# Kernel optimization log

Hardware: AMD Instinct MI355X
Metric: run time of the kernel (lower is better)

## Reference

```python
import jax, jax.numpy as jnp
import numpy as np

TAU = 1.0
EPS = 1e-8  # F.cosine_similarity default eps


def _normalize(v):
    n = jnp.sqrt(jnp.sum(v * v, axis=-1, keepdims=True))
    return v / jnp.maximum(n, EPS)


def _compute_cl(X, Y):
    # cosine-sim matrix via normalize + matmul (same math as broadcasted
    # F.cosine_similarity, without the (bs,bs,hidden) intermediate)
    S = _normalize(X) @ _normalize(Y).T            # (bs, bs), S[i,j] = cos(X_i, Y_j)
    E = jnp.exp(S / TAU)                            # (bs, bs)
    pos = jnp.diagonal(E)                           # (bs,) exp(diag/tau)
    neg = jnp.sum(E, axis=0) - pos                  # (bs,) column sums minus diagonal
    return (-jnp.log(pos / neg))[:, None]           # (bs, 1) — torch's view(bs, -1)


def setup_inputs() -> dict:
    key = jax.random.key(0)
    kx, ky = jax.random.split(key)
    X = jax.random.normal(kx, (8192, 2048), dtype=jnp.float32)
    Y = jax.random.normal(ky, (8192, 2048), dtype=jnp.float32)
    return {"X": X, "Y": Y}


def reference(X, Y):
    return _compute_cl(X, Y) + _compute_cl(Y, X)
```

## Files before the change

kernel.cpp:

```cpp
#include <hip/hip_runtime.h>
#include <hip/hip_bf16.h>
#include <math.h>

typedef float f32x4 __attribute__((ext_vector_type(4)));
typedef int   i32x4 __attribute__((ext_vector_type(4)));
typedef int   i32x8 __attribute__((ext_vector_type(8)));

#define BSZ 8192
#define DIM 2048
#define NTILE 64
#define NKG 16

#define SCALE_I32 0x79797979


__device__ __forceinline__ unsigned f2fp4(float v) {
  float a = fabsf(v);
  unsigned s = (__float_as_uint(v) >> 31) << 3;
  unsigned m = (a < 0.25f) ? 0u
             : (a < 0.75f) ? 1u
             : (a < 1.25f) ? 2u
             : (a < 1.75f) ? 3u
             : (a < 2.5f)  ? 4u
             : (a < 3.5f)  ? 5u
             : (a < 5.0f)  ? 6u : 7u;
  return s | m;
}

__global__ void __launch_bounds__(256) k_prep(const float* __restrict__ X,
                                              const float* __restrict__ Y,
                                              unsigned char* __restrict__ Xq,
                                              unsigned char* __restrict__ Yq,
                                              float* __restrict__ dg) {
  const int row = blockIdx.x;
  const int tid = threadIdx.x;
  const float4* xp = (const float4*)(X + (size_t)row * DIM);
  const float4* yp = (const float4*)(Y + (size_t)row * DIM);
  float4 x0 = xp[tid * 2], x1 = xp[tid * 2 + 1];
  float4 y0 = yp[tid * 2], y1 = yp[tid * 2 + 1];
  float sxx = x0.x*x0.x + x0.y*x0.y + x0.z*x0.z + x0.w*x0.w
            + x1.x*x1.x + x1.y*x1.y + x1.z*x1.z + x1.w*x1.w;
  float syy = y0.x*y0.x + y0.y*y0.y + y0.z*y0.z + y0.w*y0.w
            + y1.x*y1.x + y1.y*y1.y + y1.z*y1.z + y1.w*y1.w;
  float sxy = x0.x*y0.x + x0.y*y0.y + x0.z*y0.z + x0.w*y0.w
            + x1.x*y1.x + x1.y*y1.y + x1.z*y1.z + x1.w*y1.w;
#pragma unroll
  for (int m = 32; m >= 1; m >>= 1) {
    sxx += __shfl_xor(sxx, m);
    syy += __shfl_xor(syy, m);
    sxy += __shfl_xor(sxy, m);
  }
  __shared__ float sh[3][4];
  if ((tid & 63) == 0) {
    sh[0][tid >> 6] = sxx; sh[1][tid >> 6] = syy; sh[2][tid >> 6] = sxy;
  }
  __syncthreads();
  float xx = sh[0][0] + sh[0][1] + sh[0][2] + sh[0][3];
  float yy = sh[1][0] + sh[1][1] + sh[1][2] + sh[1][3];
  float xy = sh[2][0] + sh[2][1] + sh[2][2] + sh[2][3];
  float nx = fmaxf(sqrtf(xx), 1e-8f);
  float ny = fmaxf(sqrtf(yy), 1e-8f);
  float ix = 64.0f / nx, iy = 64.0f / ny;
  float vx[8] = {x0.x, x0.y, x0.z, x0.w, x1.x, x1.y, x1.z, x1.w};
  float vy[8] = {y0.x, y0.y, y0.z, y0.w, y1.x, y1.y, y1.z, y1.w};
  unsigned ux = 0, uy = 0;
#pragma unroll
  for (int i = 0; i < 8; ++i) {
    ux |= f2fp4(vx[i] * ix) << (4 * i);
    uy |= f2fp4(vy[i] * iy) << (4 * i);
  }
  const unsigned kkg = tid >> 4;
  const unsigned hi4 = (tid >> 2) & 3;
  const unsigned byt = (tid & 3) * 4;
  const unsigned R = row >> 4, lo16 = row & 15;
  const size_t addr = (((size_t)(kkg << 9) + R) << 10) + (hi4 * 16 + lo16) * 16 + byt;
  *(unsigned*)(Xq + addr) = ux;
  *(unsigned*)(Yq + addr) = uy;
  if (tid == 0) dg[row] = xy / (nx * ny);
}

__global__ void __launch_bounds__(256) k_gemm(const unsigned char* __restrict__ Xq,
                                              const unsigned char* __restrict__ Yq,
                                              float* __restrict__ rowpart,
                                              float* __restrict__ colpart) {
  const int bm = blockIdx.x & (NTILE - 1);
  const int bn = blockIdx.x >> 6;
  const int tileRow = bm * 128;
  const int tileCol = bn * 128;

  __shared__ float rsum2[2][128];
  __shared__ float csum2[2][128];

  const int tid = threadIdx.x;
  const int lane = tid & 63;
  const int w = tid >> 6;
  const int wr = w >> 1;
  const int wc = w & 1;
  const int lo = lane & 15;
  const int hi = lane >> 4;

  f32x4 acc[4][4];
#pragma unroll
  for (int m = 0; m < 4; ++m)
#pragma unroll
    for (int n = 0; n < 4; ++n) acc[m][n] = (f32x4){0.f, 0.f, 0.f, 0.f};

  const unsigned char* Ab = Xq + (((size_t)(bm * 8 + wr * 4)) << 10) + lane * 16;
  const unsigned char* Bb = Yq + (((size_t)(bn * 8 + wc * 4)) << 10) + lane * 16;

#define LOADF(da, db, g) do {                                                  \
    const unsigned char* pa_ = Ab + ((size_t)(g) << 19);                       \
    const unsigned char* pb_ = Bb + ((size_t)(g) << 19);                       \
    da[0] = *(const i32x4*)(pa_);                                              \
    da[1] = *(const i32x4*)(pa_ + 1024);                                       \
    da[2] = *(const i32x4*)(pa_ + 2048);                                       \
    da[3] = *(const i32x4*)(pa_ + 3072);                                       \
    db[0] = *(const i32x4*)(pb_);                                              \
    db[1] = *(const i32x4*)(pb_ + 1024);                                       \
    db[2] = *(const i32x4*)(pb_ + 2048);                                       \
    db[3] = *(const i32x4*)(pb_ + 3072);                                       \
  } while (0)

#define MM(aa, bb) do {                                                        \
    _Pragma("unroll")                                                          \
    for (int m_ = 0; m_ < 4; ++m_) {                                           \
      i32x8 av_ = {aa[m_][0], aa[m_][1], aa[m_][2], aa[m_][3], 0, 0, 0, 0};    \
      _Pragma("unroll")                                                        \
      for (int n_ = 0; n_ < 4; ++n_) {                                         \
        i32x8 bv_ = {bb[n_][0], bb[n_][1], bb[n_][2], bb[n_][3], 0, 0, 0, 0};  \
        acc[m_][n_] = __builtin_amdgcn_mfma_scale_f32_16x16x128_f8f6f4(        \
            av_, bv_, acc[m_][n_], 4, 4, 0, SCALE_I32, 0, SCALE_I32);          \
      }                                                                        \
    }                                                                          \
  } while (0)

  i32x4 a0[4], b0[4], a1[4], b1[4];
  LOADF(a0, b0, 0);
  for (int g = 0; g < NKG; g += 2) {
    LOADF(a1, b1, g + 1);
    MM(a0, b0);
    if (g + 2 < NKG) LOADF(a0, b0, g + 2);
    MM(a1, b1);
  }
#undef LOADF
#undef MM

  float rp[4][4];
  float cp[4];
#pragma unroll
  for (int m = 0; m < 4; ++m)
#pragma unroll
    for (int q = 0; q < 4; ++q) rp[m][q] = 0.f;
#pragma unroll
  for (int n = 0; n < 4; ++n) cp[n] = 0.f;

#pragma unroll
  for (int m = 0; m < 4; ++m)
#pragma unroll
    for (int n = 0; n < 4; ++n)
#pragma unroll
      for (int q = 0; q < 4; ++q) {
        float e = __expf(acc[m][n][q]);
        rp[m][q] += e;
        cp[n] += e;
      }

#pragma unroll
  for (int m = 0; m < 4; ++m)
#pragma unroll
    for (int q = 0; q < 4; ++q) {
      float v = rp[m][q];
      v += __shfl_xor(v, 1);
      v += __shfl_xor(v, 2);
      v += __shfl_xor(v, 4);
      v += __shfl_xor(v, 8);
      rp[m][q] = v;
    }
#pragma unroll
  for (int n = 0; n < 4; ++n) {
    float v = cp[n];
    v += __shfl_xor(v, 16);
    v += __shfl_xor(v, 32);
    cp[n] = v;
  }

  if (lo == 0) {
#pragma unroll
    for (int m = 0; m < 4; ++m)
#pragma unroll
      for (int q = 0; q < 4; ++q)
        rsum2[wc][wr * 64 + m * 16 + hi * 4 + q] = rp[m][q];
  }
  if (hi == 0) {
#pragma unroll
    for (int n = 0; n < 4; ++n)
      csum2[wr][wc * 64 + n * 16 + lo] = cp[n];
  }
  __syncthreads();

  if (tid < 128) {
    rowpart[(size_t)bn * BSZ + tileRow + tid] = rsum2[0][tid] + rsum2[1][tid];
    colpart[(size_t)bm * BSZ + tileCol + tid] = csum2[0][tid] + csum2[1][tid];
  }
}

__global__ void __launch_bounds__(256) k_final(const float* __restrict__ rowpart,
                                               const float* __restrict__ colpart,
                                               const float* __restrict__ dg,
                                               float* __restrict__ out) {
  const int k = blockIdx.x * 256 + threadIdx.x;
  float rs = 0.f, cs = 0.f;
#pragma unroll 8
  for (int s = 0; s < NTILE; ++s) {
    rs += rowpart[(size_t)s * BSZ + k];
    cs += colpart[(size_t)s * BSZ + k];
  }
  float d = dg[k];
  float p = __expf(d);
  out[k] = logf(cs - p) + logf(rs - p) - 2.0f * d;
}

extern "C" void kernel_launch(void* const* d_in, const int* in_sizes, int n_in,
                              void* d_out, int out_size, void* d_ws, size_t ws_size,
                              hipStream_t stream) {
  const float* X = (const float*)d_in[0];
  const float* Y = (const float*)d_in[1];
  float* out = (float*)d_out;

  char* ws = (char*)d_ws;
  unsigned char* Xq = (unsigned char*)ws;
  unsigned char* Yq = (unsigned char*)(ws + (size_t)BSZ * DIM / 2);
  float* diag = (float*)(ws + (size_t)BSZ * DIM);
  float* rowpart = (float*)(ws + (size_t)BSZ * DIM + BSZ * 4);
  float* colpart = (float*)(ws + (size_t)BSZ * DIM + BSZ * 4 + (size_t)NTILE * BSZ * 4);

  k_prep<<<BSZ, 256, 0, stream>>>(X, Y, Xq, Yq, diag);
  k_gemm<<<NTILE * NTILE, 256, 0, stream>>>(Xq, Yq, rowpart, colpart);
  k_final<<<BSZ / 256, 256, 0, stream>>>(rowpart, colpart, diag, out);
}
```

Baseline: 127.7 us.

## Switch FP4 GEMM to 32x32x64 scaled MFMA with matching packed layout

Replaces the 16x16x128 scaled FP4 MFMA tiles with 32x32x64 instructions, so each wave computes a 2x2 grid of 32x32 accumulators per 128-wide K group. The prep kernel's packed FP4 layout is changed to match the new operand fragment ordering (32-row groups, K split into halves). The epilogue row/column reductions and LDS indexing are rewritten for the 16-element accumulator layout. The aim is fewer MFMA issues with larger tiles and better operand reuse per instruction. The risk is a different register footprint and a more costly row-sum shuffle pattern.

```diff
diff --git a/kernel.cpp b/kernel.cpp
--- a/kernel.cpp
+++ b/kernel.cpp
@@ -2,7 +2,7 @@
 #include <hip/hip_bf16.h>
 #include <math.h>
 
-typedef float f32x4 __attribute__((ext_vector_type(4)));
+typedef float f32x16 __attribute__((ext_vector_type(16)));
 typedef int   i32x4 __attribute__((ext_vector_type(4)));
 typedef int   i32x8 __attribute__((ext_vector_type(8)));
 
@@ -69,11 +69,12 @@
     ux |= f2fp4(vx[i] * ix) << (4 * i);
     uy |= f2fp4(vy[i] * iy) << (4 * i);
   }
-  const unsigned kkg = tid >> 4;
-  const unsigned hi4 = (tid >> 2) & 3;
-  const unsigned byt = (tid & 3) * 4;
-  const unsigned R = row >> 4, lo16 = row & 15;
-  const size_t addr = (((size_t)(kkg << 9) + R) << 10) + (hi4 * 16 + lo16) * 16 + byt;
+  const unsigned g2    = tid >> 3;
+  const unsigned khalf = (tid >> 2) & 1;
+  const unsigned byt   = (tid & 3) * 4;
+  const unsigned R32 = row >> 5, lo32 = row & 31;
+  const size_t addr = (((size_t)(g2 << 8) + R32) << 10)
+                    + (khalf * 32 + lo32) * 16 + byt;
   *(unsigned*)(Xq + addr) = ux;
   *(unsigned*)(Yq + addr) = uy;
   if (tid == 0) dg[row] = xy / (nx * ny);
@@ -96,42 +97,48 @@
   const int w = tid >> 6;
   const int wr = w >> 1;
   const int wc = w & 1;
-  const int lo = lane & 15;
-  const int hi = lane >> 4;
-
-  f32x4 acc[4][4];
-#pragma unroll
-  for (int m = 0; m < 4; ++m)
-#pragma unroll
-    for (int n = 0; n < 4; ++n) acc[m][n] = (f32x4){0.f, 0.f, 0.f, 0.f};
-
-  const unsigned char* Ab = Xq + (((size_t)(bm * 8 + wr * 4)) << 10) + lane * 16;
-  const unsigned char* Bb = Yq + (((size_t)(bn * 8 + wc * 4)) << 10) + lane * 16;
+  const int l31 = lane & 31;
+  const int hi2 = lane >> 5;
+
+  f32x16 acc[2][2];
+#pragma unroll
+  for (int mi = 0; mi < 2; ++mi)
+#pragma unroll
+    for (int ni = 0; ni < 2; ++ni)
+#pragma unroll
+      for (int q = 0; q < 16; ++q) acc[mi][ni][q] = 0.f;
+
+  const unsigned char* Ab = Xq + (((size_t)(bm * 4 + wr * 2)) << 10) + lane * 16;
+  const unsigned char* Bb = Yq + (((size_t)(bn * 4 + wc * 2)) << 10) + lane * 16;
 
 #define LOADF(da, db, g) do {                                                  \
-    const unsigned char* pa_ = Ab + ((size_t)(g) << 19);                       \
-    const unsigned char* pb_ = Bb + ((size_t)(g) << 19);                       \
+    const unsigned char* pa_ = Ab + ((size_t)(2 * (g)) << 18);                 \
+    const unsigned char* pb_ = Bb + ((size_t)(2 * (g)) << 18);                 \
     da[0] = *(const i32x4*)(pa_);                                              \
     da[1] = *(const i32x4*)(pa_ + 1024);                                       \
-    da[2] = *(const i32x4*)(pa_ + 2048);                                       \
-    da[3] = *(const i32x4*)(pa_ + 3072);                                       \
+    da[2] = *(const i32x4*)(pa_ + (1 << 18));                                  \
+    da[3] = *(const i32x4*)(pa_ + (1 << 18) + 1024);                           \
     db[0] = *(const i32x4*)(pb_);                                              \
     db[1] = *(const i32x4*)(pb_ + 1024);                                       \
-    db[2] = *(const i32x4*)(pb_ + 2048);                                       \
-    db[3] = *(const i32x4*)(pb_ + 3072);                                       \
+    db[2] = *(const i32x4*)(pb_ + (1 << 18));                                  \
+    db[3] = *(const i32x4*)(pb_ + (1 << 18) + 1024);                           \
   } while (0)
 
 #define MM(aa, bb) do {                                                        \
     _Pragma("unroll")                                                          \
-    for (int m_ = 0; m_ < 4; ++m_) {                                           \
-      i32x8 av_ = {aa[m_][0], aa[m_][1], aa[m_][2], aa[m_][3], 0, 0, 0, 0};    \
+    for (int kk_ = 0; kk_ < 2; ++kk_)                                          \
       _Pragma("unroll")                                                        \
-      for (int n_ = 0; n_ < 4; ++n_) {                                         \
-        i32x8 bv_ = {bb[n_][0], bb[n_][1], bb[n_][2], bb[n_][3], 0, 0, 0, 0};  \
-        acc[m_][n_] = __builtin_amdgcn_mfma_scale_f32_16x16x128_f8f6f4(        \
-            av_, bv_, acc[m_][n_], 4, 4, 0, SCALE_I32, 0, SCALE_I32);          \
+      for (int mi_ = 0; mi_ < 2; ++mi_) {                                      \
+        i32x8 av_ = {aa[kk_*2+mi_][0], aa[kk_*2+mi_][1],                       \
+                     aa[kk_*2+mi_][2], aa[kk_*2+mi_][3], 0, 0, 0, 0};          \
+        _Pragma("unroll")                                                      \
+        for (int ni_ = 0; ni_ < 2; ++ni_) {                                    \
+          i32x8 bv_ = {bb[kk_*2+ni_][0], bb[kk_*2+ni_][1],                     \
+                       bb[kk_*2+ni_][2], bb[kk_*2+ni_][3], 0, 0, 0, 0};        \
+          acc[mi_][ni_] = __builtin_amdgcn_mfma_scale_f32_32x32x64_f8f6f4(     \
+              av_, bv_, acc[mi_][ni_], 4, 4, 0, SCALE_I32, 0, SCALE_I32);      \
+        }                                                                      \
       }                                                                        \
-    }                                                                          \
   } while (0)
 
   i32x4 a0[4], b0[4], a1[4], b1[4];
@@ -145,56 +152,53 @@
 #undef LOADF
 #undef MM
 
-  float rp[4][4];
-  float cp[4];
-#pragma unroll
-  for (int m = 0; m < 4; ++m)
-#pragma unroll
-    for (int q = 0; q < 4; ++q) rp[m][q] = 0.f;
-#pragma unroll
-  for (int n = 0; n < 4; ++n) cp[n] = 0.f;
-
-#pragma unroll
-  for (int m = 0; m < 4; ++m)
-#pragma unroll
-    for (int n = 0; n < 4; ++n)
-#pragma unroll
-      for (int q = 0; q < 4; ++q) {
-        float e = __expf(acc[m][n][q]);
-        rp[m][q] += e;
-        cp[n] += e;
+  float rp[2][16];
+  float cp[2];
+#pragma unroll
+  for (int mi = 0; mi < 2; ++mi)
+#pragma unroll
+    for (int r = 0; r < 16; ++r) rp[mi][r] = 0.f;
+  cp[0] = 0.f; cp[1] = 0.f;
+
+#pragma unroll
+  for (int mi = 0; mi < 2; ++mi)
+#pragma unroll
+    for (int ni = 0; ni < 2; ++ni)
+#pragma unroll
+      for (int r = 0; r < 16; ++r) {
+        float e = __expf(acc[mi][ni][r]);
+        rp[mi][r] += e;
+        cp[ni] += e;
       }
 
 #pragma unroll
-  for (int m = 0; m < 4; ++m)
-#pragma unroll
-    for (int q = 0; q < 4; ++q) {
-      float v = rp[m][q];
+  for (int mi = 0; mi < 2; ++mi)
+#pragma unroll
+    for (int r = 0; r < 16; ++r) {
+      float v = rp[mi][r];
       v += __shfl_xor(v, 1);
       v += __shfl_xor(v, 2);
       v += __shfl_xor(v, 4);
       v += __shfl_xor(v, 8);
-      rp[m][q] = v;
+      v += __shfl_xor(v, 16);
+      rp[mi][r] = v;
     }
-#pragma unroll
-  for (int n = 0; n < 4; ++n) {
-    float v = cp[n];
-    v += __shfl_xor(v, 16);
-    v += __shfl_xor(v, 32);
-    cp[n] = v;
-  }
-
-  if (lo == 0) {
-#pragma unroll
-    for (int m = 0; m < 4; ++m)
-#pragma unroll
-      for (int q = 0; q < 4; ++q)
-        rsum2[wc][wr * 64 + m * 16 + hi * 4 + q] = rp[m][q];
-  }
-  if (hi == 0) {
-#pragma unroll
-    for (int n = 0; n < 4; ++n)
-      csum2[wr][wc * 64 + n * 16 + lo] = cp[n];
+  cp[0] += __shfl_xor(cp[0], 32);
+  cp[1] += __shfl_xor(cp[1], 32);
+
+  if (l31 == 0) {
+#pragma unroll
+    for (int mi = 0; mi < 2; ++mi)
+#pragma unroll
+      for (int r = 0; r < 16; ++r) {
+        int lrow = wr * 64 + mi * 32 + (r & 3) + 8 * (r >> 2) + 4 * hi2;
+        rsum2[wc][lrow] = rp[mi][r];
+      }
+  }
+  if (hi2 == 0) {
+#pragma unroll
+    for (int ni = 0; ni < 2; ++ni)
+      csum2[wr][wc * 64 + ni * 32 + l31] = cp[ni];
   }
   __syncthreads();
 
```

New measurement: 139.1 us. +9.0%, slower.
